# Optimization experiments

Hardware: AMD Instinct MI355X
Metric: run time of the kernel (lower is better)

Reference implementation:

```python
import jax, jax.numpy as jnp
import numpy as np

B, S, D, F, E, K = 4, 1024, 512, 1024, 8, 2
LB_W, Z_W = 0.01, 0.001

def setup_inputs() -> dict:
    key = jax.random.key(0)
    k1, k2, k3, k4, k5 = jax.random.split(key, 5)
    std = 0.02
    x = jax.random.normal(k1, (B, S, D), dtype=jnp.float32)
    router_w = jax.random.normal(k2, (E, D), dtype=jnp.float32) * std  # nn.Linear weight [out,in]
    gate_w = jax.random.normal(k3, (E, D, F), dtype=jnp.float32) * std
    up_w = jax.random.normal(k4, (E, D, F), dtype=jnp.float32) * std
    down_w = jax.random.normal(k5, (E, F, D), dtype=jnp.float32) * std
    return {"x": x, "router_w": router_w, "gate_w": gate_w, "up_w": up_w, "down_w": down_w}

def reference(x, router_w, gate_w, up_w, down_w):
    b, s, d = x.shape
    e = router_w.shape[0]
    xf = x.reshape(-1, d)                      # [T, D]
    T = xf.shape[0]
    logits = xf @ router_w.T                   # [T, E]
    probs = jax.nn.softmax(logits, axis=-1)
    top_v, top_i = jax.lax.top_k(probs, K)     # [T, K]
    top_v = top_v / jnp.sum(top_v, axis=-1, keepdims=True)
    # combine[t, e] = sum_k top_v[t,k] * [top_i[t,k] == e]  (matches index_add_ accumulation)
    combine = jnp.zeros((T, e), dtype=xf.dtype).at[jnp.arange(T)[:, None], top_i].add(top_v)
    # SwiGLU experts, dense over E with weighted combine (same math as gather/scatter path)
    h_gate = jnp.einsum('td,edf->etf', xf, gate_w)   # [E, T, F]
    h_up = jnp.einsum('td,edf->etf', xf, up_w)       # [E, T, F]
    hidden = jax.nn.silu(h_gate) * h_up
    out = jnp.einsum('etf,efd,te->td', hidden, down_w, combine)  # [T, D]
    # auxiliary losses
    expert_mask = jax.nn.one_hot(top_i, e, dtype=jnp.float32).sum(axis=1)  # [T, E]
    f = expert_mask.sum(axis=0) / (T * K)
    P = probs.mean(axis=0)
    load_balance_loss = e * jnp.sum(f * P)
    z_loss = jnp.mean(jnp.square(jax.scipy.special.logsumexp(logits, axis=-1)))
    aux_loss = LB_W * load_balance_loss + Z_W * z_loss
    return out.reshape(b, s, d), aux_loss
```

## Files before the change

kernel.cpp:

```cpp
#include <hip/hip_runtime.h>

#define T_TOK 4096
#define D_DIM 512
#define F_DIM 1024
#define E_NUM 8
#define CAP   2048
#define BM    128
#define BN    64
#define BK    64
#define MT    (CAP/BM)
#define NT_GU (F_DIM/BN)
#define NT_DN (D_DIM/BN)
#define RB_TOK 32
#define CSTRIDE 32
#define RTR_BLOCKS (T_TOK/RB_TOK)

#define GU_HALF (BM*BK*2 + 2*BN*BK*2)
#define DN_HALF (BM*BK*2 + BN*BK*2)

typedef __bf16 bf16x8 __attribute__((ext_vector_type(8)));
typedef float  f32x4  __attribute__((ext_vector_type(4)));

__device__ __forceinline__ unsigned short f2bf(float f){
  unsigned int u = __builtin_bit_cast(unsigned int, f);
  u += 0x7FFFu + ((u >> 16) & 1u);
  return (unsigned short)(u >> 16);
}

__device__ __forceinline__ void gload16(const void* g, void* l){
  __builtin_amdgcn_global_load_lds(
      (const __attribute__((address_space(1))) unsigned int*)g,
      (__attribute__((address_space(3))) unsigned int*)l, 16, 0, 0);
}

__global__ __launch_bounds__(256) void prep_kernel(
    const float* __restrict__ x, const float* __restrict__ rw,
    const float* __restrict__ gw, const float* __restrict__ uw, const float* __restrict__ dw,
    unsigned short* __restrict__ Xg,
    unsigned short* __restrict__ gwt, unsigned short* __restrict__ uwt, unsigned short* __restrict__ dwt,
    int* __restrict__ cnt, int* __restrict__ slot_token, float* __restrict__ slot_w,
    float* __restrict__ Psum, float* __restrict__ zsum)
{
  __shared__ __align__(16) char smem[18432];
  int b = blockIdx.x;
  int tid = threadIdx.x;

  if (b >= RTR_BLOCKS){
    int tb = b - RTR_BLOCKS;
    int seg = tb >> 10;
    int r1023 = tb & 1023;
    int e = r1023 >> 7;
    int rr = r1023 & 127;
    const float* in; unsigned short* outp; int R, C, nbx;
    if (seg == 0){ in = gw; outp = gwt; R = D_DIM; C = F_DIM; nbx = F_DIM/64; }
    else if (seg == 1){ in = uw; outp = uwt; R = D_DIM; C = F_DIM; nbx = F_DIM/64; }
    else { in = dw; outp = dwt; R = F_DIM; C = D_DIM; nbx = D_DIM/64; }
    int c0 = (rr % nbx)*64, r0 = (rr / nbx)*64;
    const float* src = in + (size_t)e*R*C;
    unsigned short* dst = outp + (size_t)e*R*C;
    unsigned short* tile = (unsigned short*)smem;

    #pragma unroll
    for (int i=0;i<4;i++){
      int idx = i*256+tid;
      int rl = idx >> 4;
      int cseg = idx & 15;
      float4 v = *(const float4*)(src + (size_t)(r0+rl)*C + c0 + cseg*4);
      tile[(cseg*4+0)*68 + rl] = f2bf(v.x);
      tile[(cseg*4+1)*68 + rl] = f2bf(v.y);
      tile[(cseg*4+2)*68 + rl] = f2bf(v.z);
      tile[(cseg*4+3)*68 + rl] = f2bf(v.w);
    }
    __syncthreads();
    #pragma unroll
    for (int i=0;i<2;i++){
      int idx = i*256+tid;
      int c = idx >> 3;
      int rseg = idx & 7;
      ushort4 a = *(ushort4*)&tile[c*68 + rseg*8];
      ushort4 bq = *(ushort4*)&tile[c*68 + rseg*8 + 4];
      uint4 o;
      o.x = (unsigned)a.x  | ((unsigned)a.y<<16);
      o.y = (unsigned)a.z  | ((unsigned)a.w<<16);
      o.z = (unsigned)bq.x | ((unsigned)bq.y<<16);
      o.w = (unsigned)bq.z | ((unsigned)bq.w<<16);
      *(uint4*)(dst + (size_t)(c0+c)*R + r0 + rseg*8) = o;
    }
    return;
  }

  float* rws          = (float*)smem;
  float (*lp)[E_NUM]  = (float(*)[E_NUM])(smem+16384);
  float* lw1          = (float*)(smem+17408);
  float* lw2          = (float*)(smem+17536);
  float* llse         = (float*)(smem+17664);
  int*   li1          = (int*)(smem+17792);
  int*   li2          = (int*)(smem+17920);
  int*   lsl1         = (int*)(smem+18048);
  int*   lsl2         = (int*)(smem+18176);

  int wid = tid>>6, lane = tid&63;
  for (int i = tid; i < E_NUM*D_DIM; i += 256) rws[i] = rw[i];
  __syncthreads();

  uint4 pk[8];
  #pragma unroll
  for (int i=0;i<8;i++){
    int widx = wid*8 + i;
    int t = b*RB_TOK + widx;
    const float* xr = x + (size_t)t*D_DIM + lane*8;
    float4 xa = *(const float4*)xr;
    float4 xc = *(const float4*)(xr+4);
    pk[i].x = (unsigned)f2bf(xa.x) | ((unsigned)f2bf(xa.y)<<16);
    pk[i].y = (unsigned)f2bf(xa.z) | ((unsigned)f2bf(xa.w)<<16);
    pk[i].z = (unsigned)f2bf(xc.x) | ((unsigned)f2bf(xc.y)<<16);
    pk[i].w = (unsigned)f2bf(xc.z) | ((unsigned)f2bf(xc.w)<<16);

    float logit[E_NUM];
    #pragma unroll
    for (int e=0;e<E_NUM;e++){
      const float* wr = rws + e*D_DIM + lane*8;
      float4 wa = *(const float4*)wr;
      float4 wb = *(const float4*)(wr+4);
      float s = xa.x*wa.x + xa.y*wa.y + xa.z*wa.z + xa.w*wa.w
              + xc.x*wb.x + xc.y*wb.y + xc.z*wb.z + xc.w*wb.w;
      #pragma unroll
      for (int m=1;m<64;m<<=1) s += __shfl_xor(s, m);
      logit[e] = s;
    }
    float mx = logit[0];
    #pragma unroll
    for (int e=1;e<E_NUM;e++) mx = fmaxf(mx, logit[e]);
    float p[E_NUM]; float s = 0.f;
    #pragma unroll
    for (int e=0;e<E_NUM;e++){ p[e] = __expf(logit[e]-mx); s += p[e]; }
    float inv = 1.f/s;
    #pragma unroll
    for (int e=0;e<E_NUM;e++) p[e] *= inv;
    float lse = mx + __logf(s);
    int i1 = 0;
    #pragma unroll
    for (int e=1;e<E_NUM;e++) if (logit[e] > logit[i1]) i1 = e;
    int i2 = (i1==0) ? 1 : 0;
    #pragma unroll
    for (int e=0;e<E_NUM;e++) if (e != i1 && logit[e] > logit[i2]) i2 = e;
    if (lane == 0){
      float v1 = p[i1], v2 = p[i2];
      float invw = 1.f/(v1+v2);
      li1[widx] = i1; li2[widx] = i2;
      lw1[widx] = v1*invw; lw2[widx] = v2*invw;
      llse[widx] = lse;
      #pragma unroll
      for (int e=0;e<E_NUM;e++) lp[widx][e] = p[e];
    }
  }
  __syncthreads();

  if (tid < E_NUM){
    int e = tid, c = 0;
    #pragma unroll 4
    for (int j=0;j<RB_TOK;j++) c += (li1[j]==e) + (li2[j]==e);
    int idx = atomicAdd(&cnt[e*CSTRIDE], c);
    int tbase = b*RB_TOK;
    for (int j=0;j<RB_TOK;j++){
      if (li1[j]==e){ slot_token[e*CAP+idx] = tbase+j; slot_w[e*CAP+idx] = lw1[j]; lsl1[j] = e*CAP+idx; idx++; }
      if (li2[j]==e){ slot_token[e*CAP+idx] = tbase+j; slot_w[e*CAP+idx] = lw2[j]; lsl2[j] = e*CAP+idx; idx++; }
    }
    float ps = 0.f;
    #pragma unroll 4
    for (int j=0;j<RB_TOK;j++) ps += lp[j][e];
    atomicAdd(&Psum[e*CSTRIDE], ps);
  } else if (tid == 64){
    float zs = 0.f;
    #pragma unroll 4
    for (int j=0;j<RB_TOK;j++){ float l = llse[j]; zs += l*l; }
    atomicAdd(zsum, zs);
  }
  __syncthreads();

  #pragma unroll
  for (int i=0;i<8;i++){
    int widx = wid*8 + i;
    int s1 = lsl1[widx], s2 = lsl2[widx];
    *(uint4*)((char*)Xg + (size_t)s1*(D_DIM*2) + lane*16) = pk[i];
    *(uint4*)((char*)Xg + (size_t)s2*(D_DIM*2) + lane*16) = pk[i];
  }
}

__global__ __launch_bounds__(256) void gemm_gateup(
    const unsigned short* __restrict__ Xg, const unsigned short* __restrict__ gwt,
    const unsigned short* __restrict__ uwt,
    const int* __restrict__ cnt,
    const float* __restrict__ slot_w, unsigned short* __restrict__ H)
{
  int fid = blockIdx.x;
  int nid = (fid & 7)*(E_NUM*MT*NT_GU/8) + (fid >> 3);
  int e  = nid >> 8;
  int r  = nid & 255;
  int n0 = (r >> 4) * BN;
  int mt = r & 15;
  int c = cnt[e*CSTRIDE];
  int row0 = mt*BM;
  if (row0 >= c) return;
  int rem = c - row0;
  int offe = 0;
  #pragma unroll
  for (int i=0;i<E_NUM;i++) offe += (i < e) ? cnt[i*CSTRIDE] : 0;
  int tid = threadIdx.x, wid = tid>>6, lane = tid&63;
  __shared__ __align__(16) char arena[2*GU_HALF];

  int sub = lane>>3;
  int skb = ((lane&7)<<4) ^ (sub<<4);
  const char* asrc[4];
  #pragma unroll
  for (int i=0;i<4;i++){
    int rr = (wid*4+i)*8 + sub;
    asrc[i] = (const char*)Xg + ((size_t)e*CAP + row0 + rr)*(D_DIM*2) + skb;
  }
  const char* bgsrc[2]; const char* busrc[2];
  #pragma unroll
  for (int i=0;i<2;i++){
    int rr = (wid*2+i)*8 + sub;
    size_t rowb = ((size_t)e*F_DIM + n0 + rr) * (D_DIM*2);
    bgsrc[i] = (const char*)gwt + rowb + skb;
    busrc[i] = (const char*)uwt + rowb + skb;
  }

  f32x4 accg[4][2] = {};
  f32x4 accu[4][2] = {};
  int wm = wid>>1, wn = wid&1;

  auto STAGE = [&](int buf, int kt){
    size_t ko = (size_t)kt*BK*2;
    char* base = arena + buf*GU_HALF;
    #pragma unroll
    for (int i=0;i<4;i++)
      gload16(asrc[i]+ko, base + (wid*4+i)*1024);
    #pragma unroll
    for (int i=0;i<2;i++){
      gload16(bgsrc[i]+ko, base + BM*BK*2 + (wid*2+i)*1024);
      gload16(busrc[i]+ko, base + BM*BK*2 + BN*BK*2 + (wid*2+i)*1024);
    }
  };
  auto COMPUTE = [&](int buf){
    const char* base = arena + buf*GU_HALF;
    const char* As = base;
    const char* Bg = base + BM*BK*2;
    const char* Bu = base + BM*BK*2 + BN*BK*2;
    #pragma unroll
    for (int s=0;s<2;s++){
      int kc = s*4 + (lane>>4);
      bf16x8 a[4], bg[2], bu[2];
      #pragma unroll
      for (int m=0;m<4;m++){
        int ar = wm*64 + m*16 + (lane&15);
        a[m] = *(const bf16x8*)(As + ar*128 + ((kc<<4) ^ ((ar&7)<<4)));
      }
      #pragma unroll
      for (int n=0;n<2;n++){
        int br = wn*32 + n*16 + (lane&15);
        int bo = br*128 + ((kc<<4) ^ ((br&7)<<4));
        bg[n] = *(const bf16x8*)(Bg + bo);
        bu[n] = *(const bf16x8*)(Bu + bo);
      }
      #pragma unroll
      for (int m=0;m<4;m++){
        #pragma unroll
        for (int n=0;n<2;n++){
          accg[m][n] = __builtin_amdgcn_mfma_f32_16x16x32_bf16(a[m], bg[n], accg[m][n], 0,0,0);
          accu[m][n] = __builtin_amdgcn_mfma_f32_16x16x32_bf16(a[m], bu[n], accu[m][n], 0,0,0);
        }
      }
    }
  };

  STAGE(0, 0);
  __syncthreads();
  int cur = 0;
  for (int kt=0; kt<D_DIM/BK-1; ++kt){
    STAGE(cur^1, kt+1);
    COMPUTE(cur);
    __syncthreads();
    cur ^= 1;
  }
  COMPUTE(cur);

  #pragma unroll
  for (int m=0;m<4;m++){
    #pragma unroll
    for (int j=0;j<4;j++){
      int row = wm*64 + m*16 + ((lane>>4)<<2) + j;
      if (row < rem){
        float wgt = slot_w[e*CAP + row0 + row];
        size_t hb = (size_t)(offe + row0 + row)*F_DIM;
        #pragma unroll
        for (int n=0;n<2;n++){
          int col = n0 + wn*32 + n*16 + (lane&15);
          float g = accg[m][n][j];
          float u = accu[m][n][j];
          float h = g * (1.f/(1.f+__expf(-g))) * u * wgt;
          H[hb + col] = f2bf(h);
        }
      }
    }
  }
}

__global__ __launch_bounds__(256) void gemm_down(
    const unsigned short* __restrict__ H, const unsigned short* __restrict__ dwt,
    const int* __restrict__ cnt,
    const int* __restrict__ slot_token, float* __restrict__ out,
    const float* __restrict__ Psum, const float* __restrict__ zsum)
{
  int fid = blockIdx.x;
  int tid = threadIdx.x;
  if (fid == 0 && tid == 0){
    float lb = 0.f;
    #pragma unroll
    for (int e=0;e<E_NUM;e++){
      float f = (float)cnt[e*CSTRIDE] / (float)(T_TOK*2);
      float P = Psum[e*CSTRIDE] / (float)T_TOK;
      lb += f*P;
    }
    float z = zsum[0] / (float)T_TOK;
    out[(size_t)T_TOK*D_DIM] = 0.01f * ((float)E_NUM * lb) + 0.001f * z;
  }
  int nid = (fid & 7)*(E_NUM*MT*NT_DN/8) + (fid >> 3);
  int e  = nid >> 7;
  int r  = nid & 127;
  int n0 = (r >> 4) * BN;
  int mt = r & 15;
  int c = cnt[e*CSTRIDE];
  int row0 = mt*BM;
  if (row0 >= c) return;
  int rem = c - row0;
  int offe = 0;
  #pragma unroll
  for (int i=0;i<E_NUM;i++) offe += (i < e) ? cnt[i*CSTRIDE] : 0;
  int wid = tid>>6, lane = tid&63;
  __shared__ __align__(16) char arena[2*DN_HALF];
  int sub = lane>>3;
  int skb = ((lane&7)<<4) ^ (sub<<4);
  const char* asrc[4];
  #pragma unroll
  for (int i=0;i<4;i++){
    int rr = (wid*4+i)*8 + sub;
    asrc[i] = (const char*)H + ((size_t)offe + row0 + rr)*(F_DIM*2) + skb;
  }
  const char* bsrc[2];
  #pragma unroll
  for (int i=0;i<2;i++){
    int rr = (wid*2+i)*8 + sub;
    bsrc[i] = (const char*)dwt + ((size_t)e*D_DIM + n0 + rr)*(F_DIM*2) + skb;
  }
  f32x4 acc[4][2] = {};
  int wm = wid>>1, wn = wid&1;

  auto STAGE = [&](int buf, int kt){
    size_t ko = (size_t)kt*BK*2;
    char* base = arena + buf*DN_HALF;
    #pragma unroll
    for (int i=0;i<4;i++) gload16(asrc[i]+ko, base + (wid*4+i)*1024);
    #pragma unroll
    for (int i=0;i<2;i++) gload16(bsrc[i]+ko, base + BM*BK*2 + (wid*2+i)*1024);
  };
  auto COMPUTE = [&](int buf){
    const char* base = arena + buf*DN_HALF;
    const char* As = base;
    const char* Bs = base + BM*BK*2;
    #pragma unroll
    for (int s=0;s<2;s++){
      int kc = s*4 + (lane>>4);
      bf16x8 a[4], bb[2];
      #pragma unroll
      for (int m=0;m<4;m++){
        int ar = wm*64 + m*16 + (lane&15);
        a[m] = *(const bf16x8*)(As + ar*128 + ((kc<<4) ^ ((ar&7)<<4)));
      }
      #pragma unroll
      for (int n=0;n<2;n++){
        int br = wn*32 + n*16 + (lane&15);
        bb[n] = *(const bf16x8*)(Bs + br*128 + ((kc<<4) ^ ((br&7)<<4)));
      }
      #pragma unroll
      for (int m=0;m<4;m++){
        #pragma unroll
        for (int n=0;n<2;n++)
          acc[m][n] = __builtin_amdgcn_mfma_f32_16x16x32_bf16(a[m], bb[n], acc[m][n], 0,0,0);
      }
    }
  };

  STAGE(0, 0);
  __syncthreads();
  int cur = 0;
  for (int kt=0; kt<F_DIM/BK-1; ++kt){
    STAGE(cur^1, kt+1);
    COMPUTE(cur);
    __syncthreads();
    cur ^= 1;
  }
  COMPUTE(cur);

  #pragma unroll
  for (int m=0;m<4;m++){
    #pragma unroll
    for (int j=0;j<4;j++){
      int row = wm*64 + m*16 + ((lane>>4)<<2) + j;
      if (row < rem){
        int tok = slot_token[e*CAP + row0 + row];
        #pragma unroll
        for (int n=0;n<2;n++){
          int col = n0 + wn*32 + n*16 + (lane&15);
          atomicAdd(&out[(size_t)tok*D_DIM + col], acc[m][n][j]);
        }
      }
    }
  }
}

extern "C" void kernel_launch(void* const* d_in, const int* in_sizes, int n_in,
                              void* d_out, int out_size, void* d_ws, size_t ws_size,
                              hipStream_t stream){
  const float* x  = (const float*)d_in[0];
  const float* rw = (const float*)d_in[1];
  const float* gw = (const float*)d_in[2];
  const float* uw = (const float*)d_in[3];
  const float* dw = (const float*)d_in[4];
  float* out = (float*)d_out;

  char* w = (char*)d_ws;
  unsigned short* Xg  = (unsigned short*)w;  w += (size_t)E_NUM*CAP*D_DIM*2;
  unsigned short* gwt = (unsigned short*)w;  w += (size_t)E_NUM*D_DIM*F_DIM*2;
  unsigned short* uwt = (unsigned short*)w;  w += (size_t)E_NUM*D_DIM*F_DIM*2;
  unsigned short* dwt = (unsigned short*)w;  w += (size_t)E_NUM*F_DIM*D_DIM*2;
  unsigned short* H   = (unsigned short*)w;  w += (size_t)(T_TOK*2 + BM)*F_DIM*2;
  int*   slot_token = (int*)w;               w += (size_t)E_NUM*CAP*4;
  float* slot_w     = (float*)w;             w += (size_t)E_NUM*CAP*4;
  char* meta = w;
  int*   cnt  = (int*)w;       w += E_NUM*CSTRIDE*4;
  float* Psum = (float*)w;     w += E_NUM*CSTRIDE*4;
  float* zsum = (float*)w;     w += 128;
  size_t meta_bytes = (size_t)(w - meta);

  (void)hipMemsetAsync(d_out, 0, (size_t)out_size*sizeof(float), stream);
  (void)hipMemsetAsync(meta, 0, meta_bytes, stream);

  prep_kernel<<<RTR_BLOCKS + 3*1024, 256, 0, stream>>>(
      x, rw, gw, uw, dw, Xg, gwt, uwt, dwt, cnt, slot_token, slot_w, Psum, zsum);
  gemm_gateup<<<E_NUM*MT*NT_GU, 256, 0, stream>>>(Xg, gwt, uwt, cnt, slot_w, H);
  gemm_down<<<E_NUM*MT*NT_DN, 256, 0, stream>>>(H, dwt, cnt, slot_token, out, Psum, zsum);
}
```

Measured before the change: 193.6 us.

## Fuse fp32 weight conversion into GEMM B-tile loads, drop prep transpose pass

Removes the separate weight transpose/convert-to-bf16 pass from the prep kernel. The GEMMs now read fp32 expert weights directly, convert to bf16 in registers and write them transposed into swizzled LDS tiles through a register-staged double buffer. This avoids writing and re-reading about 25 MB of bf16 weights. In exchange each GEMM block re-reads fp32 weights (twice the bytes) once per M tile, adds conversion work and scattered LDS stores to the main loop, and loses the async global-to-LDS path for the B operand.

Result: slower. 219.3 us (+13.3%).

```diff
diff --git a/kernel.cpp b/kernel.cpp
--- a/kernel.cpp
+++ b/kernel.cpp
@@ -13,10 +13,11 @@
 #define NT_DN (D_DIM/BN)
 #define RB_TOK 32
 #define CSTRIDE 32
-#define RTR_BLOCKS (T_TOK/RB_TOK)
-
-#define GU_HALF (BM*BK*2 + 2*BN*BK*2)
-#define DN_HALF (BM*BK*2 + BN*BK*2)
+
+#define BOFF0  16384
+#define BOFF1  24576
+#define GU_BUF 32768
+#define DN_BUF 24576
 
 typedef __bf16 bf16x8 __attribute__((ext_vector_type(8)));
 typedef float  f32x4  __attribute__((ext_vector_type(4)));
@@ -26,79 +27,29 @@
   u += 0x7FFFu + ((u >> 16) & 1u);
   return (unsigned short)(u >> 16);
 }
-
+__device__ __forceinline__ unsigned pk2(float a, float b){
+  return (unsigned)f2bf(a) | ((unsigned)f2bf(b)<<16);
+}
 __device__ __forceinline__ void gload16(const void* g, void* l){
   __builtin_amdgcn_global_load_lds(
       (const __attribute__((address_space(1))) unsigned int*)g,
       (__attribute__((address_space(3))) unsigned int*)l, 16, 0, 0);
 }
-
-__global__ __launch_bounds__(256) void prep_kernel(
+__device__ __forceinline__ unsigned bswz(int col){
+  return ((unsigned)((col&7) ^ ((col>>3)&7))) << 4;
+}
+
+__global__ __launch_bounds__(256) void router_kernel(
     const float* __restrict__ x, const float* __restrict__ rw,
-    const float* __restrict__ gw, const float* __restrict__ uw, const float* __restrict__ dw,
     unsigned short* __restrict__ Xg,
-    unsigned short* __restrict__ gwt, unsigned short* __restrict__ uwt, unsigned short* __restrict__ dwt,
     int* __restrict__ cnt, int* __restrict__ slot_token, float* __restrict__ slot_w,
     float* __restrict__ Psum, float* __restrict__ zsum)
 {
-  __shared__ __align__(16) char smem[18432];
-  int b = blockIdx.x;
-  int tid = threadIdx.x;
-
-  if (b >= RTR_BLOCKS){
-    int tb = b - RTR_BLOCKS;
-    int seg = tb >> 10;
-    int r1023 = tb & 1023;
-    int e = r1023 >> 7;
-    int rr = r1023 & 127;
-    const float* in; unsigned short* outp; int R, C, nbx;
-    if (seg == 0){ in = gw; outp = gwt; R = D_DIM; C = F_DIM; nbx = F_DIM/64; }
-    else if (seg == 1){ in = uw; outp = uwt; R = D_DIM; C = F_DIM; nbx = F_DIM/64; }
-    else { in = dw; outp = dwt; R = F_DIM; C = D_DIM; nbx = D_DIM/64; }
-    int c0 = (rr % nbx)*64, r0 = (rr / nbx)*64;
-    const float* src = in + (size_t)e*R*C;
-    unsigned short* dst = outp + (size_t)e*R*C;
-    unsigned short* tile = (unsigned short*)smem;
-
-    #pragma unroll
-    for (int i=0;i<4;i++){
-      int idx = i*256+tid;
-      int rl = idx >> 4;
-      int cseg = idx & 15;
-      float4 v = *(const float4*)(src + (size_t)(r0+rl)*C + c0 + cseg*4);
-      tile[(cseg*4+0)*68 + rl] = f2bf(v.x);
-      tile[(cseg*4+1)*68 + rl] = f2bf(v.y);
-      tile[(cseg*4+2)*68 + rl] = f2bf(v.z);
-      tile[(cseg*4+3)*68 + rl] = f2bf(v.w);
-    }
-    __syncthreads();
-    #pragma unroll
-    for (int i=0;i<2;i++){
-      int idx = i*256+tid;
-      int c = idx >> 3;
-      int rseg = idx & 7;
-      ushort4 a = *(ushort4*)&tile[c*68 + rseg*8];
-      ushort4 bq = *(ushort4*)&tile[c*68 + rseg*8 + 4];
-      uint4 o;
-      o.x = (unsigned)a.x  | ((unsigned)a.y<<16);
-      o.y = (unsigned)a.z  | ((unsigned)a.w<<16);
-      o.z = (unsigned)bq.x | ((unsigned)bq.y<<16);
-      o.w = (unsigned)bq.z | ((unsigned)bq.w<<16);
-      *(uint4*)(dst + (size_t)(c0+c)*R + r0 + rseg*8) = o;
-    }
-    return;
-  }
-
-  float* rws          = (float*)smem;
-  float (*lp)[E_NUM]  = (float(*)[E_NUM])(smem+16384);
-  float* lw1          = (float*)(smem+17408);
-  float* lw2          = (float*)(smem+17536);
-  float* llse         = (float*)(smem+17664);
-  int*   li1          = (int*)(smem+17792);
-  int*   li2          = (int*)(smem+17920);
-  int*   lsl1         = (int*)(smem+18048);
-  int*   lsl2         = (int*)(smem+18176);
-
+  __shared__ float rws[E_NUM*D_DIM];
+  __shared__ float lp[RB_TOK][E_NUM];
+  __shared__ float lw1[RB_TOK], lw2[RB_TOK], llse[RB_TOK];
+  __shared__ int   li1[RB_TOK], li2[RB_TOK], lsl1[RB_TOK], lsl2[RB_TOK];
+  int b = blockIdx.x, tid = threadIdx.x;
   int wid = tid>>6, lane = tid&63;
   for (int i = tid; i < E_NUM*D_DIM; i += 256) rws[i] = rw[i];
   __syncthreads();
@@ -111,10 +62,10 @@
     const float* xr = x + (size_t)t*D_DIM + lane*8;
     float4 xa = *(const float4*)xr;
     float4 xc = *(const float4*)(xr+4);
-    pk[i].x = (unsigned)f2bf(xa.x) | ((unsigned)f2bf(xa.y)<<16);
-    pk[i].y = (unsigned)f2bf(xa.z) | ((unsigned)f2bf(xa.w)<<16);
-    pk[i].z = (unsigned)f2bf(xc.x) | ((unsigned)f2bf(xc.y)<<16);
-    pk[i].w = (unsigned)f2bf(xc.z) | ((unsigned)f2bf(xc.w)<<16);
+    pk[i].x = pk2(xa.x, xa.y);
+    pk[i].y = pk2(xa.z, xa.w);
+    pk[i].z = pk2(xc.x, xc.y);
+    pk[i].w = pk2(xc.z, xc.w);
 
     float logit[E_NUM];
     #pragma unroll
@@ -181,15 +132,14 @@
   #pragma unroll
   for (int i=0;i<8;i++){
     int widx = wid*8 + i;
-    int s1 = lsl1[widx], s2 = lsl2[widx];
-    *(uint4*)((char*)Xg + (size_t)s1*(D_DIM*2) + lane*16) = pk[i];
-    *(uint4*)((char*)Xg + (size_t)s2*(D_DIM*2) + lane*16) = pk[i];
+    *(uint4*)((char*)Xg + (size_t)lsl1[widx]*(D_DIM*2) + lane*16) = pk[i];
+    *(uint4*)((char*)Xg + (size_t)lsl2[widx]*(D_DIM*2) + lane*16) = pk[i];
   }
 }
 
 __global__ __launch_bounds__(256) void gemm_gateup(
-    const unsigned short* __restrict__ Xg, const unsigned short* __restrict__ gwt,
-    const unsigned short* __restrict__ uwt,
+    const unsigned short* __restrict__ Xg,
+    const float* __restrict__ gw, const float* __restrict__ uw,
     const int* __restrict__ cnt,
     const float* __restrict__ slot_w, unsigned short* __restrict__ H)
 {
@@ -207,7 +157,7 @@
   #pragma unroll
   for (int i=0;i<E_NUM;i++) offe += (i < e) ? cnt[i*CSTRIDE] : 0;
   int tid = threadIdx.x, wid = tid>>6, lane = tid&63;
-  __shared__ __align__(16) char arena[2*GU_HALF];
+  __shared__ __align__(1024) char arena[2*GU_BUF];
 
   int sub = lane>>3;
   int skb = ((lane&7)<<4) ^ (sub<<4);
@@ -217,36 +167,48 @@
     int rr = (wid*4+i)*8 + sub;
     asrc[i] = (const char*)Xg + ((size_t)e*CAP + row0 + rr)*(D_DIM*2) + skb;
   }
-  const char* bgsrc[2]; const char* busrc[2];
-  #pragma unroll
-  for (int i=0;i<2;i++){
-    int rr = (wid*2+i)*8 + sub;
-    size_t rowb = ((size_t)e*F_DIM + n0 + rr) * (D_DIM*2);
-    bgsrc[i] = (const char*)gwt + rowb + skb;
-    busrc[i] = (const char*)uwt + rowb + skb;
-  }
+  int d2 = tid>>3, fcq = tid&7;
+  const float* gsg = gw + (size_t)e*D_DIM*F_DIM + (size_t)(2*d2)*F_DIM + n0 + fcq*8;
+  const float* gsu = uw + (size_t)e*D_DIM*F_DIM + (size_t)(2*d2)*F_DIM + n0 + fcq*8;
 
   f32x4 accg[4][2] = {};
   f32x4 accu[4][2] = {};
   int wm = wid>>1, wn = wid&1;
 
-  auto STAGE = [&](int buf, int kt){
+  float glo[8], ghi[8], ulo[8], uhi[8];
+  auto LOADB = [&](int kt){
+    const float* pg = gsg + (size_t)kt*BK*F_DIM;
+    const float* pu = gsu + (size_t)kt*BK*F_DIM;
+    float4 a0 = *(const float4*)pg;          float4 a1 = *(const float4*)(pg+4);
+    float4 a2 = *(const float4*)(pg+F_DIM);  float4 a3 = *(const float4*)(pg+F_DIM+4);
+    float4 b0 = *(const float4*)pu;          float4 b1 = *(const float4*)(pu+4);
+    float4 b2 = *(const float4*)(pu+F_DIM);  float4 b3 = *(const float4*)(pu+F_DIM+4);
+    glo[0]=a0.x; glo[1]=a0.y; glo[2]=a0.z; glo[3]=a0.w; glo[4]=a1.x; glo[5]=a1.y; glo[6]=a1.z; glo[7]=a1.w;
+    ghi[0]=a2.x; ghi[1]=a2.y; ghi[2]=a2.z; ghi[3]=a2.w; ghi[4]=a3.x; ghi[5]=a3.y; ghi[6]=a3.z; ghi[7]=a3.w;
+    ulo[0]=b0.x; ulo[1]=b0.y; ulo[2]=b0.z; ulo[3]=b0.w; ulo[4]=b1.x; ulo[5]=b1.y; ulo[6]=b1.z; ulo[7]=b1.w;
+    uhi[0]=b2.x; uhi[1]=b2.y; uhi[2]=b2.z; uhi[3]=b2.w; uhi[4]=b3.x; uhi[5]=b3.y; uhi[6]=b3.z; uhi[7]=b3.w;
+  };
+  auto WRITEB = [&](int buf){
+    char* bg = arena + buf*GU_BUF + BOFF0;
+    char* bu = arena + buf*GU_BUF + BOFF1;
+    #pragma unroll
+    for (int j=0;j<8;j++){
+      int col = fcq*8 + j;
+      unsigned addr = ((unsigned)(col*128 + d2*4)) ^ bswz(col);
+      *(unsigned*)(bg + addr) = pk2(glo[j], ghi[j]);
+      *(unsigned*)(bu + addr) = pk2(ulo[j], uhi[j]);
+    }
+  };
+  auto LOADA = [&](int buf, int kt){
     size_t ko = (size_t)kt*BK*2;
-    char* base = arena + buf*GU_HALF;
-    #pragma unroll
-    for (int i=0;i<4;i++)
-      gload16(asrc[i]+ko, base + (wid*4+i)*1024);
-    #pragma unroll
-    for (int i=0;i<2;i++){
-      gload16(bgsrc[i]+ko, base + BM*BK*2 + (wid*2+i)*1024);
-      gload16(busrc[i]+ko, base + BM*BK*2 + BN*BK*2 + (wid*2+i)*1024);
-    }
+    char* base = arena + buf*GU_BUF;
+    #pragma unroll
+    for (int i=0;i<4;i++) gload16(asrc[i]+ko, base + (wid*4+i)*1024);
   };
   auto COMPUTE = [&](int buf){
-    const char* base = arena + buf*GU_HALF;
-    const char* As = base;
-    const char* Bg = base + BM*BK*2;
-    const char* Bu = base + BM*BK*2 + BN*BK*2;
+    const char* base = arena + buf*GU_BUF;
+    const char* Bg = base + BOFF0;
+    const char* Bu = base + BOFF1;
     #pragma unroll
     for (int s=0;s<2;s++){
       int kc = s*4 + (lane>>4);
@@ -254,14 +216,14 @@
       #pragma unroll
       for (int m=0;m<4;m++){
         int ar = wm*64 + m*16 + (lane&15);
-        a[m] = *(const bf16x8*)(As + ar*128 + ((kc<<4) ^ ((ar&7)<<4)));
+        a[m] = *(const bf16x8*)(base + ar*128 + ((kc<<4) ^ ((ar&7)<<4)));
       }
       #pragma unroll
       for (int n=0;n<2;n++){
         int br = wn*32 + n*16 + (lane&15);
-        int bo = br*128 + ((kc<<4) ^ ((br&7)<<4));
-        bg[n] = *(const bf16x8*)(Bg + bo);
-        bu[n] = *(const bf16x8*)(Bu + bo);
+        unsigned addr = ((unsigned)(br*128 + kc*16)) ^ bswz(br);
+        bg[n] = *(const bf16x8*)(Bg + addr);
+        bu[n] = *(const bf16x8*)(Bu + addr);
       }
       #pragma unroll
       for (int m=0;m<4;m++){
@@ -274,12 +236,16 @@
     }
   };
 
-  STAGE(0, 0);
+  LOADB(0);
+  LOADA(0, 0);
+  WRITEB(0);
   __syncthreads();
   int cur = 0;
   for (int kt=0; kt<D_DIM/BK-1; ++kt){
-    STAGE(cur^1, kt+1);
+    LOADB(kt+1);
+    LOADA(cur^1, kt+1);
     COMPUTE(cur);
+    WRITEB(cur^1);
     __syncthreads();
     cur ^= 1;
   }
@@ -307,7 +273,7 @@
 }
 
 __global__ __launch_bounds__(256) void gemm_down(
-    const unsigned short* __restrict__ H, const unsigned short* __restrict__ dwt,
+    const unsigned short* __restrict__ H, const float* __restrict__ dw,
     const int* __restrict__ cnt,
     const int* __restrict__ slot_token, float* __restrict__ out,
     const float* __restrict__ Psum, const float* __restrict__ zsum)
@@ -338,7 +304,8 @@
   #pragma unroll
   for (int i=0;i<E_NUM;i++) offe += (i < e) ? cnt[i*CSTRIDE] : 0;
   int wid = tid>>6, lane = tid&63;
-  __shared__ __align__(16) char arena[2*DN_HALF];
+  __shared__ __align__(1024) char arena[2*DN_BUF];
+
   int sub = lane>>3;
   int skb = ((lane&7)<<4) ^ (sub<<4);
   const char* asrc[4];
@@ -347,27 +314,38 @@
     int rr = (wid*4+i)*8 + sub;
     asrc[i] = (const char*)H + ((size_t)offe + row0 + rr)*(F_DIM*2) + skb;
   }
-  const char* bsrc[2];
-  #pragma unroll
-  for (int i=0;i<2;i++){
-    int rr = (wid*2+i)*8 + sub;
-    bsrc[i] = (const char*)dwt + ((size_t)e*D_DIM + n0 + rr)*(F_DIM*2) + skb;
-  }
+  int f2 = tid>>3, dcq = tid&7;
+  const float* gsd = dw + (size_t)e*F_DIM*D_DIM + (size_t)(2*f2)*D_DIM + n0 + dcq*8;
+
   f32x4 acc[4][2] = {};
   int wm = wid>>1, wn = wid&1;
 
-  auto STAGE = [&](int buf, int kt){
+  float dlo[8], dhi[8];
+  auto LOADB = [&](int kt){
+    const float* pd = gsd + (size_t)kt*BK*D_DIM;
+    float4 a0 = *(const float4*)pd;          float4 a1 = *(const float4*)(pd+4);
+    float4 a2 = *(const float4*)(pd+D_DIM);  float4 a3 = *(const float4*)(pd+D_DIM+4);
+    dlo[0]=a0.x; dlo[1]=a0.y; dlo[2]=a0.z; dlo[3]=a0.w; dlo[4]=a1.x; dlo[5]=a1.y; dlo[6]=a1.z; dlo[7]=a1.w;
+    dhi[0]=a2.x; dhi[1]=a2.y; dhi[2]=a2.z; dhi[3]=a2.w; dhi[4]=a3.x; dhi[5]=a3.y; dhi[6]=a3.z; dhi[7]=a3.w;
+  };
+  auto WRITEB = [&](int buf){
+    char* bs = arena + buf*DN_BUF + BOFF0;
+    #pragma unroll
+    for (int j=0;j<8;j++){
+      int col = dcq*8 + j;
+      unsigned addr = ((unsigned)(col*128 + f2*4)) ^ bswz(col);
+      *(unsigned*)(bs + addr) = pk2(dlo[j], dhi[j]);
+    }
+  };
+  auto LOADA = [&](int buf, int kt){
     size_t ko = (size_t)kt*BK*2;
-    char* base = arena + buf*DN_HALF;
+    char* base = arena + buf*DN_BUF;
     #pragma unroll
     for (int i=0;i<4;i++) gload16(asrc[i]+ko, base + (wid*4+i)*1024);
-    #pragma unroll
-    for (int i=0;i<2;i++) gload16(bsrc[i]+ko, base + BM*BK*2 + (wid*2+i)*1024);
   };
   auto COMPUTE = [&](int buf){
-    const char* base = arena + buf*DN_HALF;
-    const char* As = base;
-    const char* Bs = base + BM*BK*2;
+    const char* base = arena + buf*DN_BUF;
+    const char* Bs = base + BOFF0;
     #pragma unroll
     for (int s=0;s<2;s++){
       int kc = s*4 + (lane>>4);
@@ -375,12 +353,13 @@
       #pragma unroll
       for (int m=0;m<4;m++){
         int ar = wm*64 + m*16 + (lane&15);
-        a[m] = *(const bf16x8*)(As + ar*128 + ((kc<<4) ^ ((ar&7)<<4)));
+        a[m] = *(const bf16x8*)(base + ar*128 + ((kc<<4) ^ ((ar&7)<<4)));
       }
       #pragma unroll
       for (int n=0;n<2;n++){
         int br = wn*32 + n*16 + (lane&15);
-        bb[n] = *(const bf16x8*)(Bs + br*128 + ((kc<<4) ^ ((br&7)<<4)));
+        unsigned addr = ((unsigned)(br*128 + kc*16)) ^ bswz(br);
+        bb[n] = *(const bf16x8*)(Bs + addr);
       }
       #pragma unroll
       for (int m=0;m<4;m++){
@@ -391,12 +370,16 @@
     }
   };
 
-  STAGE(0, 0);
+  LOADB(0);
+  LOADA(0, 0);
+  WRITEB(0);
   __syncthreads();
   int cur = 0;
   for (int kt=0; kt<F_DIM/BK-1; ++kt){
-    STAGE(cur^1, kt+1);
+    LOADB(kt+1);
+    LOADA(cur^1, kt+1);
     COMPUTE(cur);
+    WRITEB(cur^1);
     __syncthreads();
     cur ^= 1;
   }
@@ -431,9 +414,6 @@
 
   char* w = (char*)d_ws;
   unsigned short* Xg  = (unsigned short*)w;  w += (size_t)E_NUM*CAP*D_DIM*2;
-  unsigned short* gwt = (unsigned short*)w;  w += (size_t)E_NUM*D_DIM*F_DIM*2;
-  unsigned short* uwt = (unsigned short*)w;  w += (size_t)E_NUM*D_DIM*F_DIM*2;
-  unsigned short* dwt = (unsigned short*)w;  w += (size_t)E_NUM*F_DIM*D_DIM*2;
   unsigned short* H   = (unsigned short*)w;  w += (size_t)(T_TOK*2 + BM)*F_DIM*2;
   int*   slot_token = (int*)w;               w += (size_t)E_NUM*CAP*4;
   float* slot_w     = (float*)w;             w += (size_t)E_NUM*CAP*4;
@@ -446,8 +426,8 @@
   (void)hipMemsetAsync(d_out, 0, (size_t)out_size*sizeof(float), stream);
   (void)hipMemsetAsync(meta, 0, meta_bytes, stream);
 
-  prep_kernel<<<RTR_BLOCKS + 3*1024, 256, 0, stream>>>(
-      x, rw, gw, uw, dw, Xg, gwt, uwt, dwt, cnt, slot_token, slot_w, Psum, zsum);
-  gemm_gateup<<<E_NUM*MT*NT_GU, 256, 0, stream>>>(Xg, gwt, uwt, cnt, slot_w, H);
-  gemm_down<<<E_NUM*MT*NT_DN, 256, 0, stream>>>(H, dwt, cnt, slot_token, out, Psum, zsum);
-}
+  router_kernel<<<T_TOK/RB_TOK, 256, 0, stream>>>(
+      x, rw, Xg, cnt, slot_token, slot_w, Psum, zsum);
+  gemm_gateup<<<E_NUM*MT*NT_GU, 256, 0, stream>>>(Xg, gw, uw, cnt, slot_w, H);
+  gemm_down<<<E_NUM*MT*NT_DN, 256, 0, stream>>>(H, dw, cnt, slot_token, out, Psum, zsum);
+}
```

## Prefetch two K-tiles ahead with partial vmcnt waits in expert GEMMs

Applied to the files above, without the earlier changes.

Both the gate/up and down-projection GEMM kernels now issue loads for tiles 0 and 1 up front. Each iteration waits only on the older tile's direct-to-LDS loads, using s_waitcnt vmcnt with a count of outstanding loads, instead of draining all loads with __syncthreads. The aim is to keep one tile of global loads in flight during compute and hide memory latency better. This relies on exact load counts per STAGE and explicit barriers and scheduling fences, so any mismatch would cause races.

Result: slower. 200.0 us (+3.3%).

```diff
diff --git a/kernel.cpp b/kernel.cpp
--- a/kernel.cpp
+++ b/kernel.cpp
@@ -244,7 +244,6 @@
   };
   auto COMPUTE = [&](int buf){
     const char* base = arena + buf*GU_HALF;
-    const char* As = base;
     const char* Bg = base + BM*BK*2;
     const char* Bu = base + BM*BK*2 + BN*BK*2;
     #pragma unroll
@@ -254,7 +253,7 @@
       #pragma unroll
       for (int m=0;m<4;m++){
         int ar = wm*64 + m*16 + (lane&15);
-        a[m] = *(const bf16x8*)(As + ar*128 + ((kc<<4) ^ ((ar&7)<<4)));
+        a[m] = *(const bf16x8*)(base + ar*128 + ((kc<<4) ^ ((ar&7)<<4)));
       }
       #pragma unroll
       for (int n=0;n<2;n++){
@@ -275,15 +274,21 @@
   };
 
   STAGE(0, 0);
-  __syncthreads();
-  int cur = 0;
-  for (int kt=0; kt<D_DIM/BK-1; ++kt){
-    STAGE(cur^1, kt+1);
-    COMPUTE(cur);
-    __syncthreads();
-    cur ^= 1;
-  }
-  COMPUTE(cur);
+  STAGE(1, 1);
+  #pragma unroll 1
+  for (int t=0; t<D_DIM/BK-1; ++t){
+    asm volatile("s_waitcnt vmcnt(8)" ::: "memory");
+    __builtin_amdgcn_s_barrier();
+    __builtin_amdgcn_sched_barrier(0);
+    COMPUTE(t & 1);
+    __builtin_amdgcn_s_barrier();
+    __builtin_amdgcn_sched_barrier(0);
+    if (t+2 < D_DIM/BK) STAGE(t & 1, t+2);
+  }
+  asm volatile("s_waitcnt vmcnt(0)" ::: "memory");
+  __builtin_amdgcn_s_barrier();
+  __builtin_amdgcn_sched_barrier(0);
+  COMPUTE((D_DIM/BK-1) & 1);
 
   #pragma unroll
   for (int m=0;m<4;m++){
@@ -366,7 +371,6 @@
   };
   auto COMPUTE = [&](int buf){
     const char* base = arena + buf*DN_HALF;
-    const char* As = base;
     const char* Bs = base + BM*BK*2;
     #pragma unroll
     for (int s=0;s<2;s++){
@@ -375,7 +379,7 @@
       #pragma unroll
       for (int m=0;m<4;m++){
         int ar = wm*64 + m*16 + (lane&15);
-        a[m] = *(const bf16x8*)(As + ar*128 + ((kc<<4) ^ ((ar&7)<<4)));
+        a[m] = *(const bf16x8*)(base + ar*128 + ((kc<<4) ^ ((ar&7)<<4)));
       }
       #pragma unroll
       for (int n=0;n<2;n++){
@@ -392,15 +396,21 @@
   };
 
   STAGE(0, 0);
-  __syncthreads();
-  int cur = 0;
-  for (int kt=0; kt<F_DIM/BK-1; ++kt){
-    STAGE(cur^1, kt+1);
-    COMPUTE(cur);
-    __syncthreads();
-    cur ^= 1;
-  }
-  COMPUTE(cur);
+  STAGE(1, 1);
+  #pragma unroll 1
+  for (int t=0; t<F_DIM/BK-1; ++t){
+    asm volatile("s_waitcnt vmcnt(6)" ::: "memory");
+    __builtin_amdgcn_s_barrier();
+    __builtin_amdgcn_sched_barrier(0);
+    COMPUTE(t & 1);
+    __builtin_amdgcn_s_barrier();
+    __builtin_amdgcn_sched_barrier(0);
+    if (t+2 < F_DIM/BK) STAGE(t & 1, t+2);
+  }
+  asm volatile("s_waitcnt vmcnt(0)" ::: "memory");
+  __builtin_amdgcn_s_barrier();
+  __builtin_amdgcn_sched_barrier(0);
+  COMPUTE((F_DIM/BK-1) & 1);
 
   #pragma unroll
   for (int m=0;m<4;m++){
```
